# Kernel tuning notes

Measured on AMD Instinct MI355X. Metric: run time of the kernel, lower is better.

The kernel has to match this reference:

```python
import jax, jax.numpy as jnp
import numpy as np

D_MODEL = 1024
N_HEADS = 16
D_HEAD = D_MODEL // N_HEADS


def setup_inputs() -> dict:
    key = jax.random.key(0)
    ks = jax.random.split(key, 6)
    query = jax.random.normal(ks[0], (2, 2048, D_MODEL), dtype=jnp.float32)
    context = jax.random.normal(ks[1], (2, 4096, D_MODEL), dtype=jnp.float32)
    s = 1.0 / np.sqrt(D_MODEL)
    Wq = jax.random.normal(ks[2], (D_MODEL, D_MODEL), dtype=jnp.float32) * s
    Wk = jax.random.normal(ks[3], (D_MODEL, D_MODEL), dtype=jnp.float32) * s
    Wv = jax.random.normal(ks[4], (D_MODEL, D_MODEL), dtype=jnp.float32) * s
    Wo = jax.random.normal(ks[5], (D_MODEL, D_MODEL), dtype=jnp.float32) * s
    return {"query": query, "context": context, "Wq": Wq, "Wk": Wk, "Wv": Wv, "Wo": Wo}


def reference(query, context, Wq, Wk, Wv, Wo):
    B, T_q, D = query.shape
    T_c = context.shape[1]
    # nn.Linear(bias=False): y = x @ W.T
    Q = (query @ Wq.T).reshape(B, T_q, N_HEADS, D_HEAD)
    K = (context @ Wk.T).reshape(B, T_c, N_HEADS, D_HEAD)
    V = (context @ Wv.T).reshape(B, T_c, N_HEADS, D_HEAD)
    scale = jnp.sqrt(jnp.asarray(D_HEAD, dtype=query.dtype))
    # non-causal cross-attention; chunking in the original is mathematically
    # identical to the full softmax attention below
    scores = jnp.einsum('bqhd,bkhd->bhqk', Q, K) / scale
    attn = jax.nn.softmax(scores, axis=-1)
    out = jnp.einsum('bhqk,bkhd->bqhd', attn, V).reshape(B, T_q, D)
    return out @ Wo.T
```

## Files before the change

### kernel.cpp

```cpp
#include <hip/hip_runtime.h>

typedef __attribute__((__ext_vector_type__(4))) float f32x4;
typedef __attribute__((__ext_vector_type__(16))) float f32x16;
typedef __attribute__((__ext_vector_type__(8))) __bf16 bf16x8;
typedef __attribute__((__ext_vector_type__(8))) unsigned short u16x8;
typedef __attribute__((__ext_vector_type__(4))) unsigned int u32x4;

#define AS1 __attribute__((address_space(1)))
#define AS3 __attribute__((address_space(3)))

__device__ __forceinline__ unsigned short f2bf(float f) {
  unsigned int u = __float_as_uint(f);
  u += 0x7FFFu + ((u >> 16) & 1u);
  return (unsigned short)(u >> 16);
}
__device__ __forceinline__ float bf2f(unsigned short u) {
  return __uint_as_float((unsigned int)u << 16);
}
__device__ __forceinline__ unsigned int packtrunc(float lo, float hi) {
  return (__float_as_uint(hi) & 0xFFFF0000u) | (__float_as_uint(lo) >> 16);
}

__global__ void cast_all(const float* __restrict__ q, const float* __restrict__ c,
                         const float* __restrict__ wq, const float* __restrict__ wk,
                         const float* __restrict__ wv, const float* __restrict__ wo,
                         unsigned short* __restrict__ qb, unsigned short* __restrict__ cb,
                         unsigned short* __restrict__ wqb, unsigned short* __restrict__ wkb,
                         unsigned short* __restrict__ wvb, unsigned short* __restrict__ wob) {
  const int blk = blockIdx.x;
  const float* s; unsigned short* d; int off;
  if (blk < 4096)        { s = q;  d = qb;  off = blk; }
  else if (blk < 12288)  { s = c;  d = cb;  off = blk - 4096; }
  else if (blk < 13312)  { s = wq; d = wqb; off = blk - 12288; }
  else if (blk < 14336)  { s = wk; d = wkb; off = blk - 13312; }
  else if (blk < 15360)  { s = wv; d = wvb; off = blk - 14336; }
  else                   { s = wo; d = wob; off = blk - 15360; }
  const long i = ((long)off * 256 + threadIdx.x) * 4;
  float4 v = *reinterpret_cast<const float4*>(s + i);
  ushort4 o;
  o.x = f2bf(v.x); o.y = f2bf(v.y); o.z = f2bf(v.z); o.w = f2bf(v.w);
  *reinterpret_cast<ushort4*>(d + i) = o;
}

__device__ __forceinline__ void gemm_core(const unsigned short* __restrict__ A,
                                          const unsigned short* __restrict__ Bt,
                                          unsigned short* As, unsigned short* Bs,
                                          int m0, int n0, f32x4 acc[4][4]) {
  const int tid = threadIdx.x, lane = tid & 63, wid = tid >> 6;
  const int fr = lane & 15, fg = lane >> 4;
  const int wr = wid >> 1, wc = wid & 1;
  const int srow = wid * 16 + (lane >> 2);
  const int scol = (lane & 3) * 8;
  const unsigned short* a0 = A + (long)(m0 + srow) * 1024 + scol;
  const unsigned short* b0 = Bt + (long)(n0 + srow) * 1024 + scol;

  for (int k0 = 0; k0 < 1024; k0 += 32) {
    __builtin_amdgcn_global_load_lds((const AS1 void*)(a0 + k0),
                                     (AS3 void*)(As + wid * 512), 16, 0, 0);
    __builtin_amdgcn_global_load_lds((const AS1 void*)(a0 + 64 * 1024 + k0),
                                     (AS3 void*)(As + 2048 + wid * 512), 16, 0, 0);
    __builtin_amdgcn_global_load_lds((const AS1 void*)(b0 + k0),
                                     (AS3 void*)(Bs + wid * 512), 16, 0, 0);
    __builtin_amdgcn_global_load_lds((const AS1 void*)(b0 + 64 * 1024 + k0),
                                     (AS3 void*)(Bs + 2048 + wid * 512), 16, 0, 0);
    __syncthreads();
    bf16x8 af[4], bfr[4];
#pragma unroll
    for (int m = 0; m < 4; ++m)
      af[m] = *reinterpret_cast<const bf16x8*>(&As[(wr * 64 + m * 16 + fr) * 32 + fg * 8]);
#pragma unroll
    for (int n = 0; n < 4; ++n)
      bfr[n] = *reinterpret_cast<const bf16x8*>(&Bs[(wc * 64 + n * 16 + fr) * 32 + fg * 8]);
#pragma unroll
    for (int m = 0; m < 4; ++m)
#pragma unroll
      for (int n = 0; n < 4; ++n)
        acc[m][n] = __builtin_amdgcn_mfma_f32_16x16x32_bf16(af[m], bfr[n], acc[m][n], 0, 0, 0);
    __syncthreads();
  }
}

__global__ __launch_bounds__(256) void proj_fused(const unsigned short* __restrict__ qb,
                                                  const unsigned short* __restrict__ cb,
                                                  const unsigned short* __restrict__ wqb,
                                                  const unsigned short* __restrict__ wkb,
                                                  const unsigned short* __restrict__ wvb,
                                                  unsigned short* __restrict__ Qb,
                                                  unsigned short* __restrict__ Kb,
                                                  unsigned short* __restrict__ Vt) {
  const int bid = blockIdx.x;
  const unsigned short *A, *Bt; unsigned short* C; int mode, loc;
  if (bid < 256)      { A = qb; Bt = wqb; C = Qb; mode = 0; loc = bid; }
  else if (bid < 768) { A = cb; Bt = wkb; C = Kb; mode = 0; loc = bid - 256; }
  else                { A = cb; Bt = wvb; C = Vt; mode = 2; loc = bid - 768; }
  const int m0 = (loc >> 3) << 7, n0 = (loc & 7) << 7;

  __shared__ __align__(16) unsigned short As[128 * 32];
  __shared__ __align__(16) unsigned short Bs[128 * 32];
  f32x4 acc[4][4];
#pragma unroll
  for (int m = 0; m < 4; ++m)
#pragma unroll
    for (int n = 0; n < 4; ++n) acc[m][n] = {0.f, 0.f, 0.f, 0.f};

  gemm_core(A, Bt, As, Bs, m0, n0, acc);

  const int lane = threadIdx.x & 63, wid = threadIdx.x >> 6;
  const int fr = lane & 15, fg = lane >> 4, wr = wid >> 1, wc = wid & 1;
  if (mode == 0) {
#pragma unroll
    for (int m = 0; m < 4; ++m) {
      const int row = m0 + wr * 64 + m * 16 + fg * 4;
#pragma unroll
      for (int n = 0; n < 4; ++n) {
        const int col = n0 + wc * 64 + n * 16 + fr;
#pragma unroll
        for (int r = 0; r < 4; ++r)
          C[(long)(row + r) * 1024 + col] = f2bf(acc[m][n][r]);
      }
    }
  } else {
#pragma unroll
    for (int m = 0; m < 4; ++m) {
      const int row = m0 + wr * 64 + m * 16 + fg * 4;
      const int bb = row >> 12, t = row & 4095;
#pragma unroll
      for (int n = 0; n < 4; ++n) {
        const int col = n0 + wc * 64 + n * 16 + fr;
        ushort4 o;
        o.x = f2bf(acc[m][n][0]); o.y = f2bf(acc[m][n][1]);
        o.z = f2bf(acc[m][n][2]); o.w = f2bf(acc[m][n][3]);
        *reinterpret_cast<ushort4*>(&C[((long)(bb * 1024 + col)) * 4096 + t]) = o;
      }
    }
  }
}

__global__ __launch_bounds__(256) void gemm_o(const unsigned short* __restrict__ A,
                                              const unsigned short* __restrict__ Bt,
                                              float* __restrict__ C) {
  const int m0 = ((int)blockIdx.x >> 3) << 7, n0 = ((int)blockIdx.x & 7) << 7;
  __shared__ __align__(16) unsigned short As[128 * 32];
  __shared__ __align__(16) unsigned short Bs[128 * 32];
  f32x4 acc[4][4];
#pragma unroll
  for (int m = 0; m < 4; ++m)
#pragma unroll
    for (int n = 0; n < 4; ++n) acc[m][n] = {0.f, 0.f, 0.f, 0.f};
  gemm_core(A, Bt, As, Bs, m0, n0, acc);
  const int lane = threadIdx.x & 63, wid = threadIdx.x >> 6;
  const int fr = lane & 15, fg = lane >> 4, wr = wid >> 1, wc = wid & 1;
#pragma unroll
  for (int m = 0; m < 4; ++m) {
    const int row = m0 + wr * 64 + m * 16 + fg * 4;
#pragma unroll
    for (int n = 0; n < 4; ++n) {
      const int col = n0 + wc * 64 + n * 16 + fr;
#pragma unroll
      for (int r = 0; r < 4; ++r)
        C[(long)(row + r) * 1024 + col] = acc[m][n][r];
    }
  }
}

#define SC 0.18033688011112042f
#define MSC 5.7707801635558535f

__global__ __launch_bounds__(256, 4) void flash_attn(const unsigned short* __restrict__ Q,
                                                     const unsigned short* __restrict__ Kb,
                                                     const unsigned short* __restrict__ Vt,
                                                     unsigned short* __restrict__ Op,
                                                     float* __restrict__ Lp) {
  const int tid = threadIdx.x, lane = tid & 63, wid = tid >> 6;
  const int blk = (int)blockIdx.x;
  const int kvh = blk & 1;
  const int qt = (blk >> 1) & 15;
  const int h = (blk >> 5) & 15;
  const int b = blk >> 9;
  const int q0 = qt * 128;
  const int l = lane & 31, hi = lane >> 5, l7 = l & 7;

  __shared__ __align__(16) unsigned short Ks[2][4096];
  __shared__ __align__(16) unsigned short Vs[2][4096];

  bf16x8 qf[4];
#pragma unroll
  for (int dk = 0; dk < 4; ++dk)
    qf[dk] = *reinterpret_cast<const bf16x8*>(
        &Q[(long)(b * 2048 + q0 + wid * 32 + l) * 1024 + h * 64 + dk * 16 + hi * 8]);

  f32x16 oacc[2];
  oacc[0] = (f32x16)(0.f); oacc[1] = (f32x16)(0.f);
  float lsum = 0.f;

  const int lr = lane >> 3;
  const int swc = (lane & 7) ^ lr;
  const unsigned short* ks0 =
      Kb + (long)(b * 4096 + kvh * 2048 + wid * 16 + lr) * 1024 + h * 64 + swc * 8;
  const unsigned short* vs0 =
      Vt + (long)((b * 16 + h) * 64 + wid * 16 + lr) * 4096 + kvh * 2048 + swc * 8;

#define STAGE(buf, t)                                                                         \
  {                                                                                           \
    const long ko = (long)(t) * 65536;                                                        \
    const int vo = (t) * 64;                                                                  \
    __builtin_amdgcn_global_load_lds((const AS1 void*)(ks0 + ko),                             \
                                     (AS3 void*)(&Ks[buf][wid * 1024]), 16, 0, 0);            \
    __builtin_amdgcn_global_load_lds((const AS1 void*)(ks0 + ko + 8 * 1024),                  \
                                     (AS3 void*)(&Ks[buf][wid * 1024 + 512]), 16, 0, 0);      \
    __builtin_amdgcn_global_load_lds((const AS1 void*)(vs0 + vo),                             \
                                     (AS3 void*)(&Vs[buf][wid * 1024]), 16, 0, 0);            \
    __builtin_amdgcn_global_load_lds((const AS1 void*)(vs0 + vo + 8 * 4096),                  \
                                     (AS3 void*)(&Vs[buf][wid * 1024 + 512]), 16, 0, 0);      \
  }

  STAGE(0, 0);

  for (int t = 0; t < 32; ++t) {
    const int cur = t & 1;
    if (t < 31) {
      STAGE(cur ^ 1, t + 1);
      asm volatile("s_waitcnt vmcnt(4)" ::: "memory");
    } else {
      asm volatile("s_waitcnt vmcnt(0)" ::: "memory");
    }
    __builtin_amdgcn_s_barrier();
    __builtin_amdgcn_sched_barrier(0);

    f32x16 s2[2];
    s2[0] = (f32x16)(0.f); s2[1] = (f32x16)(0.f);
#pragma unroll
    for (int kvb = 0; kvb < 2; ++kvb) {
#pragma unroll
      for (int dk = 0; dk < 4; ++dk) {
        const int r = kvb * 32 + l;
        bf16x8 kf = *reinterpret_cast<const bf16x8*>(
            &Ks[cur][r * 64 + (((dk * 2 + hi) ^ l7) * 8)]);
        s2[kvb] = __builtin_amdgcn_mfma_f32_32x32x16_bf16(kf, qf[dk], s2[kvb], 0, 0, 0);
      }
    }

    bf16x8 pA[4];
#pragma unroll
    for (int kvb = 0; kvb < 2; ++kvb) {
      float p[16];
      float ps = 0.f;
#pragma unroll
      for (int r = 0; r < 16; ++r) {
        p[r] = __builtin_amdgcn_exp2f(fmaf(s2[kvb][r], SC, -MSC));
        ps += p[r];
      }
      lsum += ps;
      unsigned int pk[8];
#pragma unroll
      for (int i = 0; i < 8; ++i) pk[i] = packtrunc(p[2 * i], p[2 * i + 1]);
      asm("v_permlane32_swap_b32 %0, %1" : "+v"(pk[0]), "+v"(pk[2]));
      asm("v_permlane32_swap_b32 %0, %1" : "+v"(pk[1]), "+v"(pk[3]));
      asm("v_permlane32_swap_b32 %0, %1" : "+v"(pk[4]), "+v"(pk[6]));
      asm("v_permlane32_swap_b32 %0, %1" : "+v"(pk[5]), "+v"(pk[7]));
      u32x4 w0 = {pk[0], pk[1], pk[2], pk[3]};
      u32x4 w1 = {pk[4], pk[5], pk[6], pk[7]};
      pA[kvb * 2] = __builtin_bit_cast(bf16x8, w0);
      pA[kvb * 2 + 1] = __builtin_bit_cast(bf16x8, w1);
    }

#pragma unroll
    for (int dblk = 0; dblk < 2; ++dblk) {
      const int r = dblk * 32 + l;
#pragma unroll
      for (int seg = 0; seg < 4; ++seg) {
        bf16x8 vf = *reinterpret_cast<const bf16x8*>(
            &Vs[cur][r * 64 + (((seg * 2 + hi) ^ l7) * 8)]);
        oacc[dblk] = __builtin_amdgcn_mfma_f32_32x32x16_bf16(pA[seg], vf, oacc[dblk], 0, 0, 0);
      }
    }
    __builtin_amdgcn_s_barrier();
  }

  lsum += __shfl_xor(lsum, 32);
  const float inv = 1.0f / lsum;
  if (hi == 0)
    Lp[kvh * 65536 + (b * 2048 + q0 + wid * 32 + l) * 16 + h] = lsum;
  unsigned short* Oh = Op + (long)kvh * 4194304;
#pragma unroll
  for (int reg = 0; reg < 16; ++reg) {
    const int qrow = (reg & 3) + 8 * (reg >> 2) + 4 * hi;
    const float ivr = __shfl(inv, qrow, 64);
    const long rbase = (long)(b * 2048 + q0 + wid * 32 + qrow) * 1024 + h * 64;
    Oh[rbase + l] = f2bf(oacc[0][reg] * ivr);
    Oh[rbase + 32 + l] = f2bf(oacc[1][reg] * ivr);
  }
}

__global__ void combine(const unsigned short* __restrict__ Op,
                        const float* __restrict__ Lp,
                        unsigned short* __restrict__ AO) {
  const long i = ((long)blockIdx.x * 256 + threadIdx.x) * 8;
  const int row = (int)(i >> 10);
  const int h = ((int)(i >> 6)) & 15;
  const float l0 = Lp[row * 16 + h];
  const float l1 = Lp[65536 + row * 16 + h];
  const float inv = 1.0f / (l0 + l1);
  const float w0 = l0 * inv, w1 = l1 * inv;
  u16x8 a = *reinterpret_cast<const u16x8*>(Op + i);
  u16x8 bq = *reinterpret_cast<const u16x8*>(Op + 4194304 + i);
  u16x8 o;
#pragma unroll
  for (int j = 0; j < 8; ++j)
    o[j] = f2bf(bf2f(a[j]) * w0 + bf2f(bq[j]) * w1);
  *reinterpret_cast<u16x8*>(AO + i) = o;
}

extern "C" void kernel_launch(void* const* d_in, const int* in_sizes, int n_in,
                              void* d_out, int out_size, void* d_ws, size_t ws_size,
                              hipStream_t stream) {
  const float* query = (const float*)d_in[0];
  const float* context = (const float*)d_in[1];
  const float* Wq = (const float*)d_in[2];
  const float* Wk = (const float*)d_in[3];
  const float* Wv = (const float*)d_in[4];
  const float* Wo = (const float*)d_in[5];

  char* ws = (char*)d_ws;
  unsigned short* qb = (unsigned short*)(ws);
  unsigned short* cb = (unsigned short*)(ws + 8388608);
  unsigned short* wqb = (unsigned short*)(ws + 25165824);
  unsigned short* wkb = (unsigned short*)(ws + 27262976);
  unsigned short* wvb = (unsigned short*)(ws + 29360128);
  unsigned short* wob = (unsigned short*)(ws + 31457280);
  unsigned short* Qb = (unsigned short*)(ws + 33554432);
  unsigned short* Kb = (unsigned short*)(ws + 41943040);
  unsigned short* Vt = (unsigned short*)(ws + 58720256);
  unsigned short* Op = (unsigned short*)(ws + 8388608);
  float* Lp = (float*)(ws + 25165824);
  unsigned short* AO = qb;

  cast_all<<<16384, 256, 0, stream>>>(query, context, Wq, Wk, Wv, Wo,
                                      qb, cb, wqb, wkb, wvb, wob);
  proj_fused<<<1280, 256, 0, stream>>>(qb, cb, wqb, wkb, wvb, Qb, Kb, Vt);
  flash_attn<<<1024, 256, 0, stream>>>(Qb, Kb, Vt, Op, Lp);
  combine<<<2048, 256, 0, stream>>>(Op, Lp, AO);
  gemm_o<<<256, 256, 0, stream>>>(AO, wob, (float*)d_out);
}
```

Baseline: 216.4 us.

## Register-prefetch K/V into single LDS buffer, fold softmax scale into Q projection, remap GEMM blocks

Flash attention now prefetches the next K/V tile into registers with ordinary global loads and writes it to a single LDS buffer after the compute step, in place of async global_load_lds double buffering. This halves LDS use and may raise occupancy, but it adds an extra barrier per iteration. The softmax scale is folded into the Q projection epilogue, and the MFMA accumulator is initialised with the offset so the exponent needs no per-element FMA. The projection and output GEMMs also remap block indices to interleave tiles across XCDs, which may improve cache locality.

```diff
diff --git a/kernel.cpp b/kernel.cpp
--- a/kernel.cpp
+++ b/kernel.cpp
@@ -8,6 +8,9 @@
 
 #define AS1 __attribute__((address_space(1)))
 #define AS3 __attribute__((address_space(3)))
+
+#define SC 0.18033688011112042f
+#define MSC 5.7707801635558535f
 
 __device__ __forceinline__ unsigned short f2bf(float f) {
   unsigned int u = __float_as_uint(f);
@@ -88,9 +91,11 @@
                                                   unsigned short* __restrict__ Qb,
                                                   unsigned short* __restrict__ Kb,
                                                   unsigned short* __restrict__ Vt) {
-  const int bid = blockIdx.x;
+  const int raw = blockIdx.x;
+  const int bid = (raw & 7) * 160 + (raw >> 3);
   const unsigned short *A, *Bt; unsigned short* C; int mode, loc;
-  if (bid < 256)      { A = qb; Bt = wqb; C = Qb; mode = 0; loc = bid; }
+  float oscale = 1.0f;
+  if (bid < 256)      { A = qb; Bt = wqb; C = Qb; mode = 0; loc = bid; oscale = SC; }
   else if (bid < 768) { A = cb; Bt = wkb; C = Kb; mode = 0; loc = bid - 256; }
   else                { A = cb; Bt = wvb; C = Vt; mode = 2; loc = bid - 768; }
   const int m0 = (loc >> 3) << 7, n0 = (loc & 7) << 7;
@@ -116,7 +121,7 @@
         const int col = n0 + wc * 64 + n * 16 + fr;
 #pragma unroll
         for (int r = 0; r < 4; ++r)
-          C[(long)(row + r) * 1024 + col] = f2bf(acc[m][n][r]);
+          C[(long)(row + r) * 1024 + col] = f2bf(acc[m][n][r] * oscale);
       }
     }
   } else {
@@ -139,7 +144,9 @@
 __global__ __launch_bounds__(256) void gemm_o(const unsigned short* __restrict__ A,
                                               const unsigned short* __restrict__ Bt,
                                               float* __restrict__ C) {
-  const int m0 = ((int)blockIdx.x >> 3) << 7, n0 = ((int)blockIdx.x & 7) << 7;
+  const int raw = blockIdx.x;
+  const int bid = (raw & 7) * 32 + (raw >> 3);
+  const int m0 = (bid >> 3) << 7, n0 = (bid & 7) << 7;
   __shared__ __align__(16) unsigned short As[128 * 32];
   __shared__ __align__(16) unsigned short Bs[128 * 32];
   f32x4 acc[4][4];
@@ -162,9 +169,6 @@
     }
   }
 }
-
-#define SC 0.18033688011112042f
-#define MSC 5.7707801635558535f
 
 __global__ __launch_bounds__(256, 4) void flash_attn(const unsigned short* __restrict__ Q,
                                                      const unsigned short* __restrict__ Kb,
@@ -180,8 +184,8 @@
   const int q0 = qt * 128;
   const int l = lane & 31, hi = lane >> 5, l7 = l & 7;
 
-  __shared__ __align__(16) unsigned short Ks[2][4096];
-  __shared__ __align__(16) unsigned short Vs[2][4096];
+  __shared__ __align__(16) unsigned short Ks[4096];
+  __shared__ __align__(16) unsigned short Vs[4096];
 
   bf16x8 qf[4];
 #pragma unroll
@@ -194,48 +198,43 @@
   float lsum = 0.f;
 
   const int lr = lane >> 3;
-  const int swc = (lane & 7) ^ lr;
-  const unsigned short* ks0 =
-      Kb + (long)(b * 4096 + kvh * 2048 + wid * 16 + lr) * 1024 + h * 64 + swc * 8;
-  const unsigned short* vs0 =
-      Vt + (long)((b * 16 + h) * 64 + wid * 16 + lr) * 4096 + kvh * 2048 + swc * 8;
-
-#define STAGE(buf, t)                                                                         \
-  {                                                                                           \
-    const long ko = (long)(t) * 65536;                                                        \
-    const int vo = (t) * 64;                                                                  \
-    __builtin_amdgcn_global_load_lds((const AS1 void*)(ks0 + ko),                             \
-                                     (AS3 void*)(&Ks[buf][wid * 1024]), 16, 0, 0);            \
-    __builtin_amdgcn_global_load_lds((const AS1 void*)(ks0 + ko + 8 * 1024),                  \
-                                     (AS3 void*)(&Ks[buf][wid * 1024 + 512]), 16, 0, 0);      \
-    __builtin_amdgcn_global_load_lds((const AS1 void*)(vs0 + vo),                             \
-                                     (AS3 void*)(&Vs[buf][wid * 1024]), 16, 0, 0);            \
-    __builtin_amdgcn_global_load_lds((const AS1 void*)(vs0 + vo + 8 * 4096),                  \
-                                     (AS3 void*)(&Vs[buf][wid * 1024 + 512]), 16, 0, 0);      \
-  }
-
-  STAGE(0, 0);
+  const int c8 = lane & 7;
+  const unsigned short* ksrc =
+      Kb + (long)(b * 4096 + kvh * 2048 + wid * 16 + lr) * 1024 + h * 64 + c8 * 8;
+  const unsigned short* vsrc =
+      Vt + (long)((b * 16 + h) * 64 + wid * 16 + lr) * 4096 + kvh * 2048 + c8 * 8;
+  const int wk0 = (wid * 16 + lr) * 64 + ((c8 ^ lr) * 8);
+  const int wk1 = (wid * 16 + 8 + lr) * 64 + ((c8 ^ lr) * 8);
+
+  u16x8 rk0 = *reinterpret_cast<const u16x8*>(ksrc);
+  u16x8 rk1 = *reinterpret_cast<const u16x8*>(ksrc + 8 * 1024);
+  u16x8 rv0 = *reinterpret_cast<const u16x8*>(vsrc);
+  u16x8 rv1 = *reinterpret_cast<const u16x8*>(vsrc + 8 * 4096);
+  *reinterpret_cast<u16x8*>(&Ks[wk0]) = rk0;
+  *reinterpret_cast<u16x8*>(&Ks[wk1]) = rk1;
+  *reinterpret_cast<u16x8*>(&Vs[wk0]) = rv0;
+  *reinterpret_cast<u16x8*>(&Vs[wk1]) = rv1;
+  __syncthreads();
 
   for (int t = 0; t < 32; ++t) {
-    const int cur = t & 1;
     if (t < 31) {
-      STAGE(cur ^ 1, t + 1);
-      asm volatile("s_waitcnt vmcnt(4)" ::: "memory");
-    } else {
-      asm volatile("s_waitcnt vmcnt(0)" ::: "memory");
-    }
-    __builtin_amdgcn_s_barrier();
-    __builtin_amdgcn_sched_barrier(0);
+      const long ko = (long)(t + 1) * 65536;
+      const int vo = (t + 1) * 64;
+      rk0 = *reinterpret_cast<const u16x8*>(ksrc + ko);
+      rk1 = *reinterpret_cast<const u16x8*>(ksrc + ko + 8 * 1024);
+      rv0 = *reinterpret_cast<const u16x8*>(vsrc + vo);
+      rv1 = *reinterpret_cast<const u16x8*>(vsrc + vo + 8 * 4096);
+    }
 
     f32x16 s2[2];
-    s2[0] = (f32x16)(0.f); s2[1] = (f32x16)(0.f);
+    s2[0] = (f32x16)(-MSC); s2[1] = (f32x16)(-MSC);
 #pragma unroll
     for (int kvb = 0; kvb < 2; ++kvb) {
 #pragma unroll
       for (int dk = 0; dk < 4; ++dk) {
         const int r = kvb * 32 + l;
         bf16x8 kf = *reinterpret_cast<const bf16x8*>(
-            &Ks[cur][r * 64 + (((dk * 2 + hi) ^ l7) * 8)]);
+            &Ks[r * 64 + (((dk * 2 + hi) ^ l7) * 8)]);
         s2[kvb] = __builtin_amdgcn_mfma_f32_32x32x16_bf16(kf, qf[dk], s2[kvb], 0, 0, 0);
       }
     }
@@ -247,7 +246,7 @@
       float ps = 0.f;
 #pragma unroll
       for (int r = 0; r < 16; ++r) {
-        p[r] = __builtin_amdgcn_exp2f(fmaf(s2[kvb][r], SC, -MSC));
+        p[r] = __builtin_amdgcn_exp2f(s2[kvb][r]);
         ps += p[r];
       }
       lsum += ps;
@@ -270,11 +269,19 @@
 #pragma unroll
       for (int seg = 0; seg < 4; ++seg) {
         bf16x8 vf = *reinterpret_cast<const bf16x8*>(
-            &Vs[cur][r * 64 + (((seg * 2 + hi) ^ l7) * 8)]);
+            &Vs[r * 64 + (((seg * 2 + hi) ^ l7) * 8)]);
         oacc[dblk] = __builtin_amdgcn_mfma_f32_32x32x16_bf16(pA[seg], vf, oacc[dblk], 0, 0, 0);
       }
     }
-    __builtin_amdgcn_s_barrier();
+
+    __syncthreads();
+    if (t < 31) {
+      *reinterpret_cast<u16x8*>(&Ks[wk0]) = rk0;
+      *reinterpret_cast<u16x8*>(&Ks[wk1]) = rk1;
+      *reinterpret_cast<u16x8*>(&Vs[wk0]) = rv0;
+      *reinterpret_cast<u16x8*>(&Vs[wk1]) = rv1;
+      __syncthreads();
+    }
   }
 
   lsum += __shfl_xor(lsum, 32);
```

New measurement: 200.0 us. 1.08x faster.
